# Kernel tuning notes

Hardware: AMD Instinct MI355X
Metric: run time of the kernel (lower is better)

## Reference

```python
import jax, jax.numpy as jnp
import numpy as np

B, R, C = 256, 1024, 1024
N_IDX = 64


def setup_inputs() -> dict:
    key = jax.random.key(0)
    kx, = jax.random.split(key, 1)
    x = jax.random.normal(kx, (B, R, C), dtype=jnp.float32)
    rows = jnp.arange(N_IDX, dtype=jnp.int32)
    cols = jnp.arange(N_IDX, dtype=jnp.int32)
    return {"x": x, "rows": rows, "cols": cols}


def _mute_msb(x):
    # frexp: x = m * 2**e with m in [0.5, 1). Muting the MSB of the exponent
    # (per the original: e = 0 if e > 0 else e) multiplies x by 2**(min(e,0)-e),
    # i.e. scales by 2**(-e) when e > 0, identity otherwise.
    e = jnp.frexp(x)[1]                                   # int exponent
    e = jax.lax.stop_gradient(e)
    scale = jnp.where(e > 0, jnp.exp2(-e.astype(x.dtype)), jnp.ones_like(x))
    return x * scale


def reference(x, rows, cols):
    # Boolean mask over the [R, C] plane selecting the (rows x cols) grid.
    mask = jnp.zeros((x.shape[1], x.shape[2]), dtype=bool)
    mask = mask.at[rows[:, None], cols[None, :]].set(True)
    y = _mute_msb(x)
    # Apply only on the selected grid, broadcast over batch.
    return jnp.where(mask[None, :, :], y, x)
```

## Files before the change

### kernel.cpp

```cpp
#include <hip/hip_runtime.h>
#include <hip/hip_bf16.h>


#define RR 1024
#define CC 1024

__global__ void mute_fixup_kernel(const float* __restrict__ x,
                                  const int* __restrict__ rows,
                                  const int* __restrict__ cols,
                                  float* __restrict__ out,
                                  int B, int nr, int nc) {
    int idx = blockIdx.x * blockDim.x + threadIdx.x;
    int total = B * nr * nc;
    if (idx >= total) return;

    int j = idx % nc;
    int t = idx / nc;
    int i = t % nr;
    int b = t / nr;

    int r = rows[i];
    int c = cols[j];

    size_t off = (size_t)b * (RR * CC) + (size_t)r * CC + (size_t)c;
    float v = x[off];

    unsigned u = __float_as_uint(v);
    unsigned E = (u >> 23) & 0xffu;
    float res = v;
    if (E >= 127u && E < 255u) {
        res = __uint_as_float((u & 0x807fffffu) | (126u << 23));
    }
    out[off] = res;
}

extern "C" void kernel_launch(void* const* d_in, const int* in_sizes, int n_in,
                              void* d_out, int out_size, void* d_ws, size_t ws_size,
                              hipStream_t stream) {
    const float* x   = (const float*)d_in[0];
    const int* rows  = (const int*)d_in[1];
    const int* cols  = (const int*)d_in[2];
    float* out       = (float*)d_out;

    const int nr = in_sizes[1];
    const int nc = in_sizes[2];
    const int B  = in_sizes[0] / (RR * CC);

    hipMemcpyAsync(out, x, (size_t)in_sizes[0] * sizeof(float),
                   hipMemcpyDeviceToDevice, stream);

    int total = B * nr * nc;
    int block = 256;
    int grid = (total + block - 1) / block;
    mute_fixup_kernel<<<grid, block, 0, stream>>>(x, rows, cols, out, B, nr, nc);
}
```

Measured before the change: 432.2 us.

## Fuse full copy and masked exponent mute into one vectorized streaming kernel

Replaces the device-to-device memcpy followed by a scatter fixup kernel with a single grid-stride float4 copy kernel that applies the exponent mute inline. Row and column selections are first compressed into 1024-bit bitmasks in the workspace by a small kernel, so each quad looks up its mask bits cheaply. This removes the second pass over the selected elements and the separate memcpy, at the cost of a custom copy that must match memcpy bandwidth and an extra tiny launch. The mask kernel uses one 64-thread block, so it assumes at most 64 indices.

```diff
diff --git a/kernel.cpp b/kernel.cpp
--- a/kernel.cpp
+++ b/kernel.cpp
@@ -5,52 +5,69 @@
 #define RR 1024
 #define CC 1024
 
-__global__ void mute_fixup_kernel(const float* __restrict__ x,
-                                  const int* __restrict__ rows,
-                                  const int* __restrict__ cols,
-                                  float* __restrict__ out,
-                                  int B, int nr, int nc) {
-    int idx = blockIdx.x * blockDim.x + threadIdx.x;
-    int total = B * nr * nc;
-    if (idx >= total) return;
+__global__ void build_masks_kernel(const int* __restrict__ rows,
+                                   const int* __restrict__ cols,
+                                   unsigned* __restrict__ masks,
+                                   int nr, int nc) {
+    int t = threadIdx.x;
+    if (t < 64) masks[t] = 0u;
+    __syncthreads();
+    if (t < nr) {
+        int r = rows[t];
+        atomicOr(&masks[r >> 5], 1u << (r & 31));
+    }
+    if (t < nc) {
+        int c = cols[t];
+        atomicOr(&masks[32 + (c >> 5)], 1u << (c & 31));
+    }
+}
 
-    int j = idx % nc;
-    int t = idx / nc;
-    int i = t % nr;
-    int b = t / nr;
-
-    int r = rows[i];
-    int c = cols[j];
-
-    size_t off = (size_t)b * (RR * CC) + (size_t)r * CC + (size_t)c;
-    float v = x[off];
-
-    unsigned u = __float_as_uint(v);
-    unsigned E = (u >> 23) & 0xffu;
-    float res = v;
-    if (E >= 127u && E < 255u) {
-        res = __uint_as_float((u & 0x807fffffu) | (126u << 23));
+__global__ void copy_mute_kernel(const float4* __restrict__ x,
+                                 float4* __restrict__ out,
+                                 const unsigned* __restrict__ masks,
+                                 long long nq) {
+    long long stride = (long long)gridDim.x * blockDim.x;
+    for (long long q = (long long)blockIdx.x * blockDim.x + threadIdx.x;
+         q < nq; q += stride) {
+        float4 v = x[q];
+        int r = (int)((q >> 8) & 1023);
+        unsigned rowbit  = (masks[r >> 5] >> (r & 31)) & 1u;
+        unsigned colword = masks[32 + (int)((q >> 3) & 31)];
+        unsigned colbits = (colword >> (((int)q & 7) * 4)) & 0xFu;
+        unsigned m = rowbit ? colbits : 0u;
+        if (m) {
+            float* f = reinterpret_cast<float*>(&v);
+#pragma unroll
+            for (int k = 0; k < 4; ++k) {
+                if ((m >> k) & 1u) {
+                    unsigned u = __float_as_uint(f[k]);
+                    unsigned E = (u >> 23) & 0xffu;
+                    if (E >= 127u && E < 255u)
+                        f[k] = __uint_as_float((u & 0x807fffffu) | (126u << 23));
+                }
+            }
+        }
+        out[q] = v;
     }
-    out[off] = res;
 }
 
 extern "C" void kernel_launch(void* const* d_in, const int* in_sizes, int n_in,
                               void* d_out, int out_size, void* d_ws, size_t ws_size,
                               hipStream_t stream) {
-    const float* x   = (const float*)d_in[0];
-    const int* rows  = (const int*)d_in[1];
-    const int* cols  = (const int*)d_in[2];
-    float* out       = (float*)d_out;
+    const float* x  = (const float*)d_in[0];
+    const int* rows = (const int*)d_in[1];
+    const int* cols = (const int*)d_in[2];
+    float* out      = (float*)d_out;
+    unsigned* masks = (unsigned*)d_ws;
 
     const int nr = in_sizes[1];
     const int nc = in_sizes[2];
-    const int B  = in_sizes[0] / (RR * CC);
 
-    hipMemcpyAsync(out, x, (size_t)in_sizes[0] * sizeof(float),
-                   hipMemcpyDeviceToDevice, stream);
+    build_masks_kernel<<<1, 64, 0, stream>>>(rows, cols, masks, nr, nc);
 
-    int total = B * nr * nc;
+    long long nq = (long long)in_sizes[0] / 4;
     int block = 256;
-    int grid = (total + block - 1) / block;
-    mute_fixup_kernel<<<grid, block, 0, stream>>>(x, rows, cols, out, B, nr, nc);
+    int grid = 2048;
+    copy_mute_kernel<<<grid, block, 0, stream>>>(
+        (const float4*)x, (float4*)out, masks, nq);
 }
```

After: 459.2 us. +6.2%, slower.
